# Performance work log

Measured on AMD Instinct MI355X. Metric: run time of the kernel, lower is better.

## Reference

```python
import jax, jax.numpy as jnp
import numpy as np

N = 50000      # nodes
E = 800000     # edges (before self loops)
F_IN = 50      # PPI num_features
H = 4          # heads
C = 64         # hidden per head
NC = 121       # PPI num_classes
NEG_SLOPE = 0.2


def setup_inputs() -> dict:
    key = jax.random.key(0)
    ks = jax.random.split(key, 20)
    p = lambda k, shape: (jax.random.normal(k, shape, jnp.float32) * 0.1)
    x0 = jax.random.normal(ks[0], (N, F_IN), jnp.float32)
    edge_index = jax.random.randint(ks[1], (2, E), 0, N, dtype=jnp.int64)
    return dict(
        x0=x0, edge_index=edge_index,
        W1=p(ks[2], (F_IN, H * C)), as1=p(ks[3], (H, C)), ad1=p(ks[4], (H, C)),
        res1=p(ks[5], (F_IN, H * C)), b1=jnp.zeros((H * C,), jnp.float32),
        W2=p(ks[6], (H * C, H * C)), as2=p(ks[7], (H, C)), ad2=p(ks[8], (H, C)),
        res2=p(ks[9], (H * C, H * C)), b2=jnp.zeros((H * C,), jnp.float32),
        W3=p(ks[10], (H * C, H * NC)), as3=p(ks[11], (H, NC)), ad3=p(ks[12], (H, NC)),
        res3=p(ks[13], (H * C, NC)), b3=jnp.zeros((NC,), jnp.float32),
    )


def _gat(x, src, dst, W, a_src, a_dst, resW, b, concat):
    """PyG-style GATConv with residual, self loops already in (src, dst)."""
    n = x.shape[0]
    heads, outc = a_src.shape
    h = (x @ W).reshape(n, heads, outc)                 # [N,H,C]
    al_s = (h * a_src).sum(-1)                          # [N,H]
    al_d = (h * a_dst).sum(-1)                          # [N,H]
    e = jax.nn.leaky_relu(al_s[src] + al_d[dst], NEG_SLOPE)  # [E,H]
    m = jax.ops.segment_max(e, dst, num_segments=n)     # stable softmax per dst
    ex = jnp.exp(e - m[dst])
    denom = jax.ops.segment_sum(ex, dst, num_segments=n)
    alpha = ex / denom[dst]                             # [E,H]
    out = jax.ops.segment_sum(h[src] * alpha[:, :, None], dst, num_segments=n)  # [N,H,C]
    out = out.reshape(n, heads * outc) if concat else out.mean(axis=1)
    return out + x @ resW + b


def reference(x0, edge_index,
              W1, as1, ad1, res1, b1,
              W2, as2, ad2, res2, b2,
              W3, as3, ad3, res3, b3):
    n = x0.shape[0]
    loop = jnp.arange(n, dtype=edge_index.dtype)        # add self loops (PyG default)
    src = jnp.concatenate([edge_index[0], loop])
    dst = jnp.concatenate([edge_index[1], loop])
    x1 = jax.nn.relu(_gat(x0, src, dst, W1, as1, ad1, res1, b1, True))
    x2 = jax.nn.relu(_gat(x1, src, dst, W2, as2, ad2, res2, b2, True))
    x3 = _gat(x2, src, dst, W3, as3, ad3, res3, b3, False)
    return x3
```

## Files before the change

kernel.cpp:

```cpp
#include <hip/hip_runtime.h>

#define NNODES 50000
#define NEDGES 800000
#define NTOT   (NEDGES + NNODES)
#define F_IN   50
#define KPAD1  64
#define HEADS  4
#define C1     64
#define HC1    256
#define NC     121
#define K1S    320
#define K3S    1280
#define N2S    512
#define SLOTS  128

typedef unsigned short ushort_t;
typedef __attribute__((ext_vector_type(4))) unsigned short ushort4_t;
typedef __attribute__((ext_vector_type(8))) unsigned short ushort8;
typedef __attribute__((ext_vector_type(8))) __bf16 bf16x8;
typedef __attribute__((ext_vector_type(4))) float f32x4;
typedef __attribute__((ext_vector_type(4))) int int4_t;

__device__ __forceinline__ ushort_t f2bf(float f) {
    union { float f; unsigned int u; } v; v.f = f;
    unsigned int u = v.u;
    return (ushort_t)((u + 0x7fffu + ((u >> 16) & 1u)) >> 16);
}
__device__ __forceinline__ float bf2f(ushort_t s) {
    union { unsigned int u; float f; } v; v.u = ((unsigned int)s) << 16;
    return v.f;
}
__device__ __forceinline__ float lrelu(float x) { return x > 0.f ? x : 0.2f * x; }
__device__ __forceinline__ f32x4 cvt4lo(ushort8 v) {
    f32x4 r; r[0] = bf2f(v[0]); r[1] = bf2f(v[1]); r[2] = bf2f(v[2]); r[3] = bf2f(v[3]);
    return r;
}
__device__ __forceinline__ f32x4 cvt4hi(ushort8 v) {
    f32x4 r; r[0] = bf2f(v[4]); r[1] = bf2f(v[5]); r[2] = bf2f(v[6]); r[3] = bf2f(v[7]);
    return r;
}
__device__ __forceinline__ void wave_lds_sync() {
    asm volatile("s_waitcnt lgkmcnt(0)" ::: "memory");
}

__device__ __forceinline__ void scatter_body(int i, const int* __restrict__ ei,
                                             int* __restrict__ cnt,
                                             int* __restrict__ csr_src) {
    if (i >= NTOT) return;
    int s, d;
    if (i < NEDGES) { s = ei[i]; d = ei[NEDGES + i]; }
    else            { s = d = i - NEDGES; }
    if ((unsigned)d >= NNODES) d = 0;
    if ((unsigned)s >= NNODES) s = 0;
    int k = atomicAdd(&cnt[d], 1);
    if (k < SLOTS) csr_src[d * SLOTS + k] = s;
}

#define SZ_A (NNODES * KPAD1)
#define SZ_B (HC1 * K1S)
#define SZ_C (N2S * HC1)
#define SZ_D (N2S)
#define SZ_E (NC * K3S)
#define SZ_F (KPAD1 * 4)
#define SZ_G (HC1 * 4)
#define PREP_TOTAL (SZ_A + SZ_B + SZ_C + SZ_D + SZ_E + 2 * SZ_F + 4 * SZ_G)
#define PREP_BLK ((PREP_TOTAL + 255) / 256)
#define CNT_BLK  ((NTOT + 255) / 256)

__device__ void prep_body(int i,
                 const float* __restrict__ x0,
                 const float* __restrict__ W1, const float* __restrict__ res1,
                 const float* __restrict__ W2, const float* __restrict__ res2,
                 const float* __restrict__ W3, const float* __restrict__ res3,
                 const float* __restrict__ as1, const float* __restrict__ ad1,
                 const float* __restrict__ as2, const float* __restrict__ ad2,
                 const float* __restrict__ as3, const float* __restrict__ ad3,
                 const float* __restrict__ b2,
                 ushort_t* __restrict__ x0b, ushort_t* __restrict__ Bt1,
                 ushort_t* __restrict__ Bt2, ushort_t* __restrict__ Bt3,
                 float* __restrict__ bias512,
                 float* __restrict__ w_as1, float* __restrict__ w_ad1,
                 float* __restrict__ w_as2, float* __restrict__ w_ad2,
                 float* __restrict__ w_as3, float* __restrict__ w_ad3) {
    if (i < SZ_A) {
        int m = i >> 6, k = i & 63;
        x0b[i] = (k < F_IN) ? f2bf(x0[(size_t)m * F_IN + k]) : (ushort_t)0;
        return;
    }
    i -= SZ_A;
    if (i < SZ_B) {
        int c = i / K1S, kk = i - c * K1S;
        float v = 0.f;
        if (kk < 256) {
            int h = kk >> 6, k = kk & 63;
            if (k < F_IN && (c >> 6) == h) v = W1[(size_t)k * HC1 + c];
        } else {
            int k = kk - 256;
            if (k < F_IN) v = res1[(size_t)k * HC1 + c];
        }
        Bt1[i] = f2bf(v);
        return;
    }
    i -= SZ_B;
    if (i < SZ_C) {
        int c = i / HC1, k = i - c * HC1;
        float v = (c < HC1) ? W2[(size_t)k * HC1 + c] : res2[(size_t)k * HC1 + (c - HC1)];
        Bt2[i] = f2bf(v);
        return;
    }
    i -= SZ_C;
    if (i < SZ_D) {
        bias512[i] = (i < HC1) ? 0.f : b2[i - HC1];
        return;
    }
    i -= SZ_D;
    if (i < SZ_E) {
        int c = i / K3S, kk = i - c * K3S;
        float v;
        if (kk < 1024) {
            int h = kk >> 8, k = kk & 255;
            v = 0.25f * W3[(size_t)k * (HEADS * NC) + h * NC + c];
        } else {
            int k = kk - 1024;
            v = res3[(size_t)k * NC + c];
        }
        Bt3[i] = f2bf(v);
        return;
    }
    i -= SZ_E;
    if (i < 2 * SZ_F) {
        const float* a = (i < SZ_F) ? as1 : ad1;
        float* w = (i < SZ_F) ? w_as1 : w_ad1;
        int ii = (i < SZ_F) ? i : i - SZ_F;
        int k = ii >> 2, h = ii & 3;
        float s = 0.f;
        if (k < F_IN)
            for (int c = 0; c < C1; ++c) s += W1[(size_t)k * HC1 + h * C1 + c] * a[h * C1 + c];
        w[ii] = s;
        return;
    }
    i -= 2 * SZ_F;
    {
        int grp = i / SZ_G, ii = i - grp * SZ_G;
        int k = ii >> 2, h = ii & 3;
        float s = 0.f;
        if (grp < 2) {
            const float* a = grp ? ad2 : as2;
            for (int c = 0; c < C1; ++c) s += W2[(size_t)k * HC1 + h * C1 + c] * a[h * C1 + c];
            (grp ? w_ad2 : w_as2)[ii] = s;
        } else {
            const float* a = (grp == 3) ? ad3 : as3;
            for (int c = 0; c < NC; ++c) s += W3[(size_t)k * (HEADS * NC) + h * NC + c] * a[h * NC + c];
            ((grp == 3) ? w_ad3 : w_as3)[ii] = s;
        }
    }
}

__global__ __launch_bounds__(256)
void prep_scatter_kernel(const float* __restrict__ x0,
                 const float* __restrict__ W1, const float* __restrict__ res1,
                 const float* __restrict__ W2, const float* __restrict__ res2,
                 const float* __restrict__ W3, const float* __restrict__ res3,
                 const float* __restrict__ as1, const float* __restrict__ ad1,
                 const float* __restrict__ as2, const float* __restrict__ ad2,
                 const float* __restrict__ as3, const float* __restrict__ ad3,
                 const float* __restrict__ b2,
                 ushort_t* __restrict__ x0b, ushort_t* __restrict__ Bt1,
                 ushort_t* __restrict__ Bt2, ushort_t* __restrict__ Bt3,
                 float* __restrict__ bias512,
                 float* __restrict__ w_as1, float* __restrict__ w_ad1,
                 float* __restrict__ w_as2, float* __restrict__ w_ad2,
                 float* __restrict__ w_as3, float* __restrict__ w_ad3,
                 const int* __restrict__ ei, int* __restrict__ cnt,
                 int* __restrict__ csr_src) {
    int b = blockIdx.x;
    if (b < PREP_BLK) {
        prep_body(b * 256 + threadIdx.x, x0, W1, res1, W2, res2, W3, res3,
                  as1, ad1, as2, ad2, as3, ad3, b2, x0b, Bt1, Bt2, Bt3,
                  bias512, w_as1, w_ad1, w_as2, w_ad2, w_as3, w_ad3);
    } else {
        scatter_body((b - PREP_BLK) * 256 + threadIdx.x, ei, cnt, csr_src);
    }
}

#define BM 128
#define BN 128
#define BK 64
#define LDP (BK + 8)

__global__ __launch_bounds__(256)
void gemm_mfma_kernel(const ushort_t* __restrict__ A1, int lda1,
                      const ushort_t* __restrict__ A2, int lda2, int Ksplit,
                      const ushort_t* __restrict__ Bt, const float* __restrict__ bias,
                      float* __restrict__ Cf, ushort_t* __restrict__ Cb,
                      int M, int N, int K, int relu) {
    __shared__ ushort_t As[BM * LDP];
    __shared__ ushort_t Bs[BN * LDP];
    int tid = threadIdx.x;
    int lane = tid & 63;
    int wid = tid >> 6;
    int wm = (wid & 1) * 64, wn = (wid >> 1) * 64;
    int l15 = lane & 15;
    int q8 = (lane >> 4) * 8;
    int m0 = blockIdx.y * BM, n0 = blockIdx.x * BN;

    f32x4 acc[4][4] = {};

    for (int k0 = 0; k0 < K; k0 += BK) {
        #pragma unroll
        for (int it = 0; it < 4; ++it) {
            int c = tid + it * 256;
            int row = c >> 3, c8 = c & 7;
            int k = k0 + c8 * 8;
            ushort8 va = (ushort8)0;
            int gm = m0 + row;
            if (gm < M) {
                if (k < Ksplit) va = *(const ushort8*)&A1[(size_t)gm * lda1 + k];
                else            va = *(const ushort8*)&A2[(size_t)gm * lda2 + (k - Ksplit)];
            }
            *(ushort8*)&As[row * LDP + c8 * 8] = va;
            ushort8 vb = (ushort8)0;
            int gn = n0 + row;
            if (gn < N) vb = *(const ushort8*)&Bt[(size_t)gn * K + k];
            *(ushort8*)&Bs[row * LDP + c8 * 8] = vb;
        }
        __syncthreads();
        #pragma unroll
        for (int kk = 0; kk < BK; kk += 32) {
            bf16x8 af[4], bfr[4];
            #pragma unroll
            for (int mi = 0; mi < 4; ++mi)
                af[mi] = *(const bf16x8*)&As[(wm + mi * 16 + l15) * LDP + kk + q8];
            #pragma unroll
            for (int ni = 0; ni < 4; ++ni)
                bfr[ni] = *(const bf16x8*)&Bs[(wn + ni * 16 + l15) * LDP + kk + q8];
            #pragma unroll
            for (int mi = 0; mi < 4; ++mi)
                #pragma unroll
                for (int ni = 0; ni < 4; ++ni)
                    acc[mi][ni] = __builtin_amdgcn_mfma_f32_16x16x32_bf16(
                        af[mi], bfr[ni], acc[mi][ni], 0, 0, 0);
        }
        __syncthreads();
    }

    #pragma unroll
    for (int mi = 0; mi < 4; ++mi) {
        int mbase = m0 + wm + mi * 16 + (lane >> 4) * 4;
        #pragma unroll
        for (int ni = 0; ni < 4; ++ni) {
            int ncol = n0 + wn + ni * 16 + l15;
            if (ncol >= N) continue;
            float bv = bias ? bias[ncol] : 0.f;
            #pragma unroll
            for (int r = 0; r < 4; ++r) {
                int m = mbase + r;
                if (m >= M) continue;
                float v = acc[mi][ni][r] + bv;
                if (relu) v = fmaxf(v, 0.f);
                if (Cf) Cf[(size_t)m * N + ncol] = v;
                else    Cb[(size_t)m * N + ncol] = f2bf(v);
            }
        }
    }
}

__global__ __launch_bounds__(256)
void gemm3s_kernel(const ushort_t* __restrict__ A1, int lda1,
                   const ushort_t* __restrict__ A2, int lda2, int Ksplit,
                   const ushort_t* __restrict__ Bt, const float* __restrict__ bias,
                   float* __restrict__ out, int M, int N, int K) {
    __shared__ ushort_t As[64 * LDP];
    __shared__ ushort_t Bs[128 * LDP];
    int tid = threadIdx.x, lane = tid & 63, wid = tid >> 6;
    int l15 = lane & 15, q8 = (lane >> 4) * 8;
    int m0 = blockIdx.x * 64;
    f32x4 c4[8] = {};
    for (int k0 = 0; k0 < K; k0 += BK) {
        #pragma unroll
        for (int it = 0; it < 2; ++it) {
            int c = tid + it * 256;
            int row = c >> 3, c8 = c & 7;
            int k = k0 + c8 * 8;
            ushort8 va = (ushort8)0;
            int gm = m0 + row;
            if (gm < M) {
                if (k < Ksplit) va = *(const ushort8*)&A1[(size_t)gm * lda1 + k];
                else            va = *(const ushort8*)&A2[(size_t)gm * lda2 + (k - Ksplit)];
            }
            *(ushort8*)&As[row * LDP + c8 * 8] = va;
        }
        #pragma unroll
        for (int it = 0; it < 4; ++it) {
            int c = tid + it * 256;
            int row = c >> 3, c8 = c & 7;
            int k = k0 + c8 * 8;
            ushort8 vb = (ushort8)0;
            if (row < N) vb = *(const ushort8*)&Bt[(size_t)row * K + k];
            *(ushort8*)&Bs[row * LDP + c8 * 8] = vb;
        }
        __syncthreads();
        #pragma unroll
        for (int kk = 0; kk < BK; kk += 32) {
            bf16x8 af = *(const bf16x8*)&As[(wid * 16 + l15) * LDP + kk + q8];
            #pragma unroll
            for (int ni = 0; ni < 8; ++ni) {
                bf16x8 bf = *(const bf16x8*)&Bs[(ni * 16 + l15) * LDP + kk + q8];
                c4[ni] = __builtin_amdgcn_mfma_f32_16x16x32_bf16(af, bf, c4[ni], 0, 0, 0);
            }
        }
        __syncthreads();
    }
    int rbase = m0 + wid * 16 + (lane >> 4) * 4;
    #pragma unroll
    for (int ni = 0; ni < 8; ++ni) {
        int col = ni * 16 + l15;
        if (col >= NC) continue;
        float bv = bias[col];
        #pragma unroll
        for (int r = 0; r < 4; ++r) {
            int m = rbase + r;
            if (m < M) out[(size_t)m * NC + col] = c4[ni][r] + bv;
        }
    }
}

__global__ __launch_bounds__(256)
void logits_gemv_kernel(const ushort_t* __restrict__ X, int K,
                        const float* __restrict__ w_as, const float* __restrict__ w_ad,
                        float* __restrict__ als, float* __restrict__ ald) {
    int wid = threadIdx.x >> 6, lane = threadIdx.x & 63;
    int n = blockIdx.x * 4 + wid;
    float ps[HEADS] = {}, pd[HEADS] = {};
    for (int k0 = lane * 4; k0 < K; k0 += 256) {
        ushort4_t xv = *(const ushort4_t*)&X[(size_t)n * K + k0];
        float x[4] = {bf2f(xv.x), bf2f(xv.y), bf2f(xv.z), bf2f(xv.w)};
        #pragma unroll
        for (int j = 0; j < 4; ++j) {
            #pragma unroll
            for (int h = 0; h < HEADS; ++h) {
                ps[h] += x[j] * w_as[(k0 + j) * 4 + h];
                pd[h] += x[j] * w_ad[(k0 + j) * 4 + h];
            }
        }
    }
    #pragma unroll
    for (int off = 32; off; off >>= 1)
        #pragma unroll
        for (int h = 0; h < HEADS; ++h) {
            ps[h] += __shfl_xor(ps[h], off);
            pd[h] += __shfl_xor(pd[h], off);
        }
    if (lane == 0)
        #pragma unroll
        for (int h = 0; h < HEADS; ++h) {
            als[n * HEADS + h] = ps[h];
            ald[n * HEADS + h] = pd[h];
        }
}

#define E_CHUNK32(ROWBYTES)                                                   \
    int i = base + l;                                                         \
    int nv = end - base; if (nv > 32) nv = 32;                                \
    if (i < end) {                                                            \
        int s = csr_src[i];                                                   \
        soffw[l] = s * (ROWBYTES);                                            \
        f32x4 av = *(const f32x4*)&als[s * 4];                                \
        f32x4 e;                                                              \
        _Pragma("unroll")                                                     \
        for (int h = 0; h < HEADS; ++h) {                                     \
            e[h] = __expf(lrelu(av[h] + aldd[h]));                            \
            den4[h] += e[h];                                                  \
        }                                                                     \
        *(f32x4*)&sew[l * 4] = e;                                             \
    }                                                                         \
    wave_lds_sync();

#define DEN_REDUCE16                                                          \
    _Pragma("unroll")                                                         \
    for (int off = 16; off; off >>= 1)                                        \
        _Pragma("unroll")                                                     \
        for (int h = 0; h < HEADS; ++h)                                       \
            den4[h] += __shfl_xor(den4[h], off);

__global__ __launch_bounds__(256)
void agg1_kernel(const ushort_t* __restrict__ x0b,
                 const float* __restrict__ als, const float* __restrict__ ald,
                 const int* __restrict__ cnt, const int* __restrict__ csr_src,
                 ushort_t* __restrict__ aggx) {
    __shared__ int   soff[8][32];
    __shared__ float se[8][32 * 4];
    int tid = threadIdx.x;
    int hw = tid >> 5, l = tid & 31;
    int d = blockIdx.x * 8 + hw;
    int* soffw = soff[hw];
    float* sew = se[hw];
    int beg = d * SLOTS;
    int deg = cnt[d]; if (deg > SLOTS) deg = SLOTS;
    int end = beg + deg;
    f32x4 aldd = *(const f32x4*)&ald[d * 4];
    f32x4 den4 = (f32x4)0.f;
    f32x4 acc0 = (f32x4)0.f, acc1 = (f32x4)0.f;
    int lb = l * 4;
    for (int base = beg; base < end; base += 32) {
        E_CHUNK32(KPAD1 * 2)
        int j = 0;
        for (; j + 4 <= nv; j += 4) {
            int4_t o = *(const int4_t*)&soffw[j];
            f32x4 e0 = *(const f32x4*)&sew[j * 4];
            f32x4 e1 = *(const f32x4*)&sew[(j + 1) * 4];
            f32x4 e2 = *(const f32x4*)&sew[(j + 2) * 4];
            f32x4 e3 = *(const f32x4*)&sew[(j + 3) * 4];
            unsigned int v0 = *(const unsigned int*)((const char*)x0b + o.x + lb);
            unsigned int v1 = *(const unsigned int*)((const char*)x0b + o.y + lb);
            unsigned int v2 = *(const unsigned int*)((const char*)x0b + o.z + lb);
            unsigned int v3 = *(const unsigned int*)((const char*)x0b + o.w + lb);
            acc0 += e0 * bf2f((ushort_t)(v0 & 0xffffu)) + e1 * bf2f((ushort_t)(v1 & 0xffffu))
                  + e2 * bf2f((ushort_t)(v2 & 0xffffu)) + e3 * bf2f((ushort_t)(v3 & 0xffffu));
            acc1 += e0 * bf2f((ushort_t)(v0 >> 16)) + e1 * bf2f((ushort_t)(v1 >> 16))
                  + e2 * bf2f((ushort_t)(v2 >> 16)) + e3 * bf2f((ushort_t)(v3 >> 16));
        }
        for (; j < nv; ++j) {
            int o = soffw[j];
            f32x4 e = *(const f32x4*)&sew[j * 4];
            unsigned int v = *(const unsigned int*)((const char*)x0b + o + lb);
            acc0 += e * bf2f((ushort_t)(v & 0xffffu));
            acc1 += e * bf2f((ushort_t)(v >> 16));
        }
        wave_lds_sync();
    }
    DEN_REDUCE16
    #pragma unroll
    for (int h = 0; h < HEADS; ++h) {
        float r = 1.f / den4[h];
        unsigned int pk = (unsigned int)f2bf(acc0[h] * r)
                        | ((unsigned int)f2bf(acc1[h] * r) << 16);
        *(unsigned int*)&aggx[(size_t)d * HC1 + h * 64 + l * 2] = pk;
    }
}

__global__ __launch_bounds__(256)
void agg2_kernel(const ushort_t* __restrict__ comb,
                 const float* __restrict__ als, const float* __restrict__ ald,
                 const int* __restrict__ cnt, const int* __restrict__ csr_src,
                 const float* __restrict__ w_as3, const float* __restrict__ w_ad3,
                 ushort_t* __restrict__ xnext,
                 float* __restrict__ als3, float* __restrict__ ald3) {
    __shared__ int   soff[8][32];
    __shared__ float se[8][32 * 4];
    int tid = threadIdx.x;
    int hw = tid >> 5, l = tid & 31;
    int d = blockIdx.x * 8 + hw;
    int* soffw = soff[hw];
    float* sew = se[hw];
    int hh = l >> 3;
    int beg = d * SLOTS;
    int deg = cnt[d]; if (deg > SLOTS) deg = SLOTS;
    int end = beg + deg;
    f32x4 aldd = *(const f32x4*)&ald[d * 4];
    f32x4 den4 = (f32x4)0.f;
    f32x4 acc[2] = {};
    int lb = l * 16;
    for (int base = beg; base < end; base += 32) {
        E_CHUNK32(N2S * 2)
        int j = 0;
        for (; j + 4 <= nv; j += 4) {
            int4_t o = *(const int4_t*)&soffw[j];
            ushort8 v0 = *(const ushort8*)((const char*)comb + o.x + lb);
            ushort8 v1 = *(const ushort8*)((const char*)comb + o.y + lb);
            ushort8 v2 = *(const ushort8*)((const char*)comb + o.z + lb);
            ushort8 v3 = *(const ushort8*)((const char*)comb + o.w + lb);
            float e0 = sew[j * 4 + hh], e1 = sew[(j + 1) * 4 + hh];
            float e2 = sew[(j + 2) * 4 + hh], e3 = sew[(j + 3) * 4 + hh];
            acc[0] += e0 * cvt4lo(v0) + e1 * cvt4lo(v1) + e2 * cvt4lo(v2) + e3 * cvt4lo(v3);
            acc[1] += e0 * cvt4hi(v0) + e1 * cvt4hi(v1) + e2 * cvt4hi(v2) + e3 * cvt4hi(v3);
        }
        for (; j < nv; ++j) {
            int o = soffw[j];
            float e = sew[j * 4 + hh];
            ushort8 v = *(const ushort8*)((const char*)comb + o + lb);
            acc[0] += e * cvt4lo(v);
            acc[1] += e * cvt4hi(v);
        }
        wave_lds_sync();
    }
    DEN_REDUCE16
    float r = 1.f / den4[hh];
    ushort8 rv = *(const ushort8*)&comb[(size_t)d * N2S + 256 + l * 8];
    float vout[8];
    ushort8 o8;
    #pragma unroll
    for (int q = 0; q < 2; ++q)
        #pragma unroll
        for (int c = 0; c < 4; ++c) {
            float vv = fmaxf(acc[q][c] * r + bf2f(rv[q * 4 + c]), 0.f);
            vout[q * 4 + c] = vv;
            o8[q * 4 + c] = f2bf(vv);
        }
    *(ushort8*)&xnext[(size_t)d * HC1 + l * 8] = o8;
    f32x4 ps = (f32x4)0.f, pd = (f32x4)0.f;
    #pragma unroll
    for (int cc = 0; cc < 8; ++cc) {
        int col = l * 8 + cc;
        f32x4 wsj = *(const f32x4*)&w_as3[col * 4];
        f32x4 wdj = *(const f32x4*)&w_ad3[col * 4];
        ps += vout[cc] * wsj;
        pd += vout[cc] * wdj;
    }
    #pragma unroll
    for (int off = 16; off; off >>= 1) {
        #pragma unroll
        for (int h = 0; h < HEADS; ++h) {
            ps[h] += __shfl_xor(ps[h], off);
            pd[h] += __shfl_xor(pd[h], off);
        }
    }
    if (l == 0) {
        *(f32x4*)&als3[d * 4] = ps;
        *(f32x4*)&ald3[d * 4] = pd;
    }
}

__global__ __launch_bounds__(256)
void agg3_kernel(const ushort_t* __restrict__ x2b,
                 const float* __restrict__ als, const float* __restrict__ ald,
                 const int* __restrict__ cnt, const int* __restrict__ csr_src,
                 ushort_t* __restrict__ aggx) {
    __shared__ int   soff[8][32];
    __shared__ float se[8][32 * 4];
    int tid = threadIdx.x;
    int hw = tid >> 5, l = tid & 31;
    int d = blockIdx.x * 8 + hw;
    int* soffw = soff[hw];
    float* sew = se[hw];
    int beg = d * SLOTS;
    int deg = cnt[d]; if (deg > SLOTS) deg = SLOTS;
    int end = beg + deg;
    f32x4 aldd = *(const f32x4*)&ald[d * 4];
    f32x4 den4 = (f32x4)0.f;
    f32x4 acc[HEADS][2] = {};
    int lb = l * 16;
    for (int base = beg; base < end; base += 32) {
        E_CHUNK32(HC1 * 2)
        int j = 0;
        for (; j + 4 <= nv; j += 4) {
            int4_t o = *(const int4_t*)&soffw[j];
            ushort8 v0 = *(const ushort8*)((const char*)x2b + o.x + lb);
            ushort8 v1 = *(const ushort8*)((const char*)x2b + o.y + lb);
            ushort8 v2 = *(const ushort8*)((const char*)x2b + o.z + lb);
            ushort8 v3 = *(const ushort8*)((const char*)x2b + o.w + lb);
            f32x4 e0 = *(const f32x4*)&sew[j * 4];
            f32x4 e1 = *(const f32x4*)&sew[(j + 1) * 4];
            f32x4 e2 = *(const f32x4*)&sew[(j + 2) * 4];
            f32x4 e3 = *(const f32x4*)&sew[(j + 3) * 4];
            f32x4 xl, xh;
            xl = cvt4lo(v0); xh = cvt4hi(v0);
            #pragma unroll
            for (int h = 0; h < HEADS; ++h) { acc[h][0] += e0[h] * xl; acc[h][1] += e0[h] * xh; }
            xl = cvt4lo(v1); xh = cvt4hi(v1);
            #pragma unroll
            for (int h = 0; h < HEADS; ++h) { acc[h][0] += e1[h] * xl; acc[h][1] += e1[h] * xh; }
            xl = cvt4lo(v2); xh = cvt4hi(v2);
            #pragma unroll
            for (int h = 0; h < HEADS; ++h) { acc[h][0] += e2[h] * xl; acc[h][1] += e2[h] * xh; }
            xl = cvt4lo(v3); xh = cvt4hi(v3);
            #pragma unroll
            for (int h = 0; h < HEADS; ++h) { acc[h][0] += e3[h] * xl; acc[h][1] += e3[h] * xh; }
        }
        for (; j < nv; ++j) {
            int o = soffw[j];
            f32x4 e = *(const f32x4*)&sew[j * 4];
            ushort8 v = *(const ushort8*)((const char*)x2b + o + lb);
            f32x4 xl = cvt4lo(v), xh = cvt4hi(v);
            #pragma unroll
            for (int h = 0; h < HEADS; ++h) { acc[h][0] += e[h] * xl; acc[h][1] += e[h] * xh; }
        }
        wave_lds_sync();
    }
    DEN_REDUCE16
    #pragma unroll
    for (int h = 0; h < HEADS; ++h) {
        float rdv = 1.f / den4[h];
        ushort8 ow;
        #pragma unroll
        for (int q = 0; q < 2; ++q)
            #pragma unroll
            for (int c = 0; c < 4; ++c)
                ow[q * 4 + c] = f2bf(acc[h][q][c] * rdv);
        *(ushort8*)&aggx[(size_t)d * 1024 + h * HC1 + l * 8] = ow;
    }
}

extern "C" void kernel_launch(void* const* d_in, const int* in_sizes, int n_in,
                              void* d_out, int out_size, void* d_ws, size_t ws_size,
                              hipStream_t stream) {
    const float* x0   = (const float*)d_in[0];
    const int*   ei   = (const int*)d_in[1];
    const float* W1   = (const float*)d_in[2];
    const float* as1  = (const float*)d_in[3];
    const float* ad1  = (const float*)d_in[4];
    const float* res1 = (const float*)d_in[5];
    const float* b1   = (const float*)d_in[6];
    const float* W2   = (const float*)d_in[7];
    const float* as2  = (const float*)d_in[8];
    const float* ad2  = (const float*)d_in[9];
    const float* res2 = (const float*)d_in[10];
    const float* b2   = (const float*)d_in[11];
    const float* W3   = (const float*)d_in[12];
    const float* as3  = (const float*)d_in[13];
    const float* ad3  = (const float*)d_in[14];
    const float* res3 = (const float*)d_in[15];
    const float* b3   = (const float*)d_in[16];

    char* p = (char*)d_ws;
    auto alloc = [&](size_t bytes) -> void* {
        void* r = (void*)p;
        p += (bytes + 255) & ~(size_t)255;
        return r;
    };
    int*      cnt     = (int*)alloc((size_t)NNODES * 4);
    int*      csr_src = (int*)alloc((size_t)NNODES * SLOTS * 4);
    float*    als     = (float*)alloc((size_t)NNODES * HEADS * 4);
    float*    ald     = (float*)alloc((size_t)NNODES * HEADS * 4);
    float*    als3    = (float*)alloc((size_t)NNODES * HEADS * 4);
    float*    ald3    = (float*)alloc((size_t)NNODES * HEADS * 4);
    ushort_t* x0b     = (ushort_t*)alloc((size_t)NNODES * KPAD1 * 2);
    ushort_t* x2      = (ushort_t*)alloc((size_t)NNODES * HC1 * 2);
    ushort_t* Bt1     = (ushort_t*)alloc((size_t)HC1 * K1S * 2);
    ushort_t* Bt2     = (ushort_t*)alloc((size_t)N2S * HC1 * 2);
    float*    bias512 = (float*)alloc((size_t)N2S * 4);
    ushort_t* Bt3     = (ushort_t*)alloc((size_t)NC * K3S * 2);
    float*    w_as1   = (float*)alloc((size_t)KPAD1 * 4 * 4);
    float*    w_ad1   = (float*)alloc((size_t)KPAD1 * 4 * 4);
    float*    w_as2   = (float*)alloc((size_t)HC1 * 4 * 4);
    float*    w_ad2   = (float*)alloc((size_t)HC1 * 4 * 4);
    float*    w_as3   = (float*)alloc((size_t)HC1 * 4 * 4);
    float*    w_ad3   = (float*)alloc((size_t)HC1 * 4 * 4);
    char*     big     = (char*)alloc((size_t)NNODES * 1024 * 2);
    ushort_t* aggx1   = (ushort_t*)big;
    ushort_t* x1      = (ushort_t*)(big + (size_t)NNODES * HC1 * 2);
    ushort_t* comb    = (ushort_t*)(big + (size_t)NNODES * HC1 * 4);
    ushort_t* aggx3   = (ushort_t*)big;

    hipMemsetAsync(cnt, 0, (size_t)NNODES * 4, stream);

    prep_scatter_kernel<<<PREP_BLK + CNT_BLK, 256, 0, stream>>>(
        x0, W1, res1, W2, res2, W3, res3, as1, ad1, as2, ad2, as3, ad3, b2,
        x0b, Bt1, Bt2, Bt3, bias512, w_as1, w_ad1, w_as2, w_ad2, w_as3, w_ad3,
        ei, cnt, csr_src);

    auto gemm = [&](const ushort_t* A1, int lda1, const ushort_t* A2, int lda2, int Ksplit,
                    const ushort_t* Bt, const float* bias,
                    float* Cf, ushort_t* Cb, int M, int Nn, int K, int relu) {
        dim3 g((Nn + BN - 1) / BN, (M + BM - 1) / BM);
        gemm_mfma_kernel<<<g, 256, 0, stream>>>(A1, lda1, A2, lda2, Ksplit, Bt, bias,
                                                Cf, Cb, M, Nn, K, relu);
    };

    int nagg4 = NNODES / 4;
    int nagg8 = NNODES / 8;

    logits_gemv_kernel<<<nagg4, 256, 0, stream>>>(x0b, KPAD1, w_as1, w_ad1, als, ald);
    agg1_kernel<<<nagg8, 256, 0, stream>>>(x0b, als, ald, cnt, csr_src, aggx1);
    gemm(aggx1, HC1, x0b, KPAD1, HC1, Bt1, b1, nullptr, x1, NNODES, HC1, K1S, 1);

    gemm(x1, HC1, x1, HC1, HC1, Bt2, bias512, nullptr, comb, NNODES, N2S, HC1, 0);
    logits_gemv_kernel<<<nagg4, 256, 0, stream>>>(x1, HC1, w_as2, w_ad2, als, ald);
    agg2_kernel<<<nagg8, 256, 0, stream>>>(comb, als, ald, cnt, csr_src,
                                           w_as3, w_ad3, x2, als3, ald3);

    agg3_kernel<<<nagg8, 256, 0, stream>>>(x2, als3, ald3, cnt, csr_src, aggx3);
    gemm3s_kernel<<<(NNODES + 63) / 64, 256, 0, stream>>>(
        aggx3, 1024, x2, HC1, 1024, Bt3, b3, (float*)d_out, NNODES, 128, K3S);
}
```

Measured before the change: 591.5 us.

## Split layer-2/3 aggregation into column stripes with edges spread across lanes

The layer-2 and layer-3 aggregation kernels now launch eight blocks per group of nodes. Each block handles a 32-column stripe, and the lanes of a half-wave split into 8 edge groups of 4 column lanes, with a shuffle reduction at the end. This is meant to raise parallelism and memory-level concurrency for gathered rows. The price is recomputing the per-edge softmax weights eight times, extra shuffles, and a new partial-logit buffer plus a small reduce kernel to build the layer-3 attention logits.

```diff
diff --git a/kernel.cpp b/kernel.cpp
--- a/kernel.cpp
+++ b/kernel.cpp
@@ -440,97 +440,117 @@
 }
 
 __global__ __launch_bounds__(256)
-void agg2_kernel(const ushort_t* __restrict__ comb,
-                 const float* __restrict__ als, const float* __restrict__ ald,
-                 const int* __restrict__ cnt, const int* __restrict__ csr_src,
-                 const float* __restrict__ w_as3, const float* __restrict__ w_ad3,
-                 ushort_t* __restrict__ xnext,
-                 float* __restrict__ als3, float* __restrict__ ald3) {
+void agg2s_kernel(const ushort_t* __restrict__ comb,
+                  const float* __restrict__ als, const float* __restrict__ ald,
+                  const int* __restrict__ cnt, const int* __restrict__ csr_src,
+                  const float* __restrict__ w_as3, const float* __restrict__ w_ad3,
+                  ushort_t* __restrict__ xnext, float* __restrict__ pbuf) {
     __shared__ int   soff[8][32];
     __shared__ float se[8][32 * 4];
     int tid = threadIdx.x;
     int hw = tid >> 5, l = tid & 31;
-    int d = blockIdx.x * 8 + hw;
+    int gb = blockIdx.x;
+    int stripe = gb & 7;
+    int d = (gb >> 3) * 8 + hw;
     int* soffw = soff[hw];
     float* sew = se[hw];
-    int hh = l >> 3;
+    int hh = stripe >> 1;
     int beg = d * SLOTS;
     int deg = cnt[d]; if (deg > SLOTS) deg = SLOTS;
     int end = beg + deg;
     f32x4 aldd = *(const f32x4*)&ald[d * 4];
     f32x4 den4 = (f32x4)0.f;
     f32x4 acc[2] = {};
-    int lb = l * 16;
+    int cg = l & 3;
+    int eg = l >> 2;
+    int lb = stripe * 64 + cg * 16;
     for (int base = beg; base < end; base += 32) {
         E_CHUNK32(N2S * 2)
-        int j = 0;
-        for (; j + 4 <= nv; j += 4) {
-            int4_t o = *(const int4_t*)&soffw[j];
-            ushort8 v0 = *(const ushort8*)((const char*)comb + o.x + lb);
-            ushort8 v1 = *(const ushort8*)((const char*)comb + o.y + lb);
-            ushort8 v2 = *(const ushort8*)((const char*)comb + o.z + lb);
-            ushort8 v3 = *(const ushort8*)((const char*)comb + o.w + lb);
-            float e0 = sew[j * 4 + hh], e1 = sew[(j + 1) * 4 + hh];
-            float e2 = sew[(j + 2) * 4 + hh], e3 = sew[(j + 3) * 4 + hh];
-            acc[0] += e0 * cvt4lo(v0) + e1 * cvt4lo(v1) + e2 * cvt4lo(v2) + e3 * cvt4lo(v3);
-            acc[1] += e0 * cvt4hi(v0) + e1 * cvt4hi(v1) + e2 * cvt4hi(v2) + e3 * cvt4hi(v3);
-        }
-        for (; j < nv; ++j) {
-            int o = soffw[j];
-            float e = sew[j * 4 + hh];
-            ushort8 v = *(const ushort8*)((const char*)comb + o + lb);
-            acc[0] += e * cvt4lo(v);
-            acc[1] += e * cvt4hi(v);
+        for (int j = 0; j < nv; j += 8) {
+            int le = j + eg;
+            if (le < nv) {
+                int o = soffw[le];
+                float e = sew[le * 4 + hh];
+                ushort8 v = *(const ushort8*)((const char*)comb + o + lb);
+                acc[0] += e * cvt4lo(v);
+                acc[1] += e * cvt4hi(v);
+            }
         }
         wave_lds_sync();
     }
     DEN_REDUCE16
-    float r = 1.f / den4[hh];
-    ushort8 rv = *(const ushort8*)&comb[(size_t)d * N2S + 256 + l * 8];
-    float vout[8];
-    ushort8 o8;
     #pragma unroll
-    for (int q = 0; q < 2; ++q)
-        #pragma unroll
-        for (int c = 0; c < 4; ++c) {
-            float vv = fmaxf(acc[q][c] * r + bf2f(rv[q * 4 + c]), 0.f);
-            vout[q * 4 + c] = vv;
-            o8[q * 4 + c] = f2bf(vv);
-        }
-    *(ushort8*)&xnext[(size_t)d * HC1 + l * 8] = o8;
+    for (int off = 4; off <= 16; off <<= 1)
+        #pragma unroll
+        for (int q = 0; q < 2; ++q)
+            #pragma unroll
+            for (int c = 0; c < 4; ++c)
+                acc[q][c] += __shfl_xor(acc[q][c], off);
+    if (eg == 0) {
+        float r = 1.f / den4[hh];
+        ushort8 rv = *(const ushort8*)&comb[(size_t)d * N2S + 256 + stripe * 32 + cg * 8];
+        float vout[8];
+        ushort8 o8;
+        #pragma unroll
+        for (int q = 0; q < 2; ++q)
+            #pragma unroll
+            for (int c = 0; c < 4; ++c) {
+                float vv = fmaxf(acc[q][c] * r + bf2f(rv[q * 4 + c]), 0.f);
+                vout[q * 4 + c] = vv;
+                o8[q * 4 + c] = f2bf(vv);
+            }
+        *(ushort8*)&xnext[(size_t)d * HC1 + stripe * 32 + cg * 8] = o8;
+        f32x4 ps = (f32x4)0.f, pd = (f32x4)0.f;
+        #pragma unroll
+        for (int cc = 0; cc < 8; ++cc) {
+            int col = stripe * 32 + cg * 8 + cc;
+            ps += vout[cc] * (*(const f32x4*)&w_as3[col * 4]);
+            pd += vout[cc] * (*(const f32x4*)&w_ad3[col * 4]);
+        }
+        #pragma unroll
+        for (int off = 1; off <= 2; off <<= 1) {
+            #pragma unroll
+            for (int h = 0; h < HEADS; ++h) {
+                ps[h] += __shfl_xor(ps[h], off);
+                pd[h] += __shfl_xor(pd[h], off);
+            }
+        }
+        if (cg == 0) {
+            float* pb = &pbuf[((size_t)stripe * NNODES + d) * 8];
+            *(f32x4*)pb = ps;
+            *(f32x4*)(pb + 4) = pd;
+        }
+    }
+}
+
+__global__ __launch_bounds__(256)
+void logits3_reduce_kernel(const float* __restrict__ pbuf,
+                           float* __restrict__ als3, float* __restrict__ ald3) {
+    int d = blockIdx.x * 256 + threadIdx.x;
+    if (d >= NNODES) return;
     f32x4 ps = (f32x4)0.f, pd = (f32x4)0.f;
     #pragma unroll
-    for (int cc = 0; cc < 8; ++cc) {
-        int col = l * 8 + cc;
-        f32x4 wsj = *(const f32x4*)&w_as3[col * 4];
-        f32x4 wdj = *(const f32x4*)&w_ad3[col * 4];
-        ps += vout[cc] * wsj;
-        pd += vout[cc] * wdj;
-    }
-    #pragma unroll
-    for (int off = 16; off; off >>= 1) {
-        #pragma unroll
-        for (int h = 0; h < HEADS; ++h) {
-            ps[h] += __shfl_xor(ps[h], off);
-            pd[h] += __shfl_xor(pd[h], off);
-        }
-    }
-    if (l == 0) {
-        *(f32x4*)&als3[d * 4] = ps;
-        *(f32x4*)&ald3[d * 4] = pd;
-    }
-}
-
-__global__ __launch_bounds__(256)
-void agg3_kernel(const ushort_t* __restrict__ x2b,
-                 const float* __restrict__ als, const float* __restrict__ ald,
-                 const int* __restrict__ cnt, const int* __restrict__ csr_src,
-                 ushort_t* __restrict__ aggx) {
+    for (int s = 0; s < 8; ++s) {
+        const float* pb = &pbuf[((size_t)s * NNODES + d) * 8];
+        ps += *(const f32x4*)pb;
+        pd += *(const f32x4*)(pb + 4);
+    }
+    *(f32x4*)&als3[d * 4] = ps;
+    *(f32x4*)&ald3[d * 4] = pd;
+}
+
+__global__ __launch_bounds__(256)
+void agg3s_kernel(const ushort_t* __restrict__ x2b,
+                  const float* __restrict__ als, const float* __restrict__ ald,
+                  const int* __restrict__ cnt, const int* __restrict__ csr_src,
+                  ushort_t* __restrict__ aggx) {
     __shared__ int   soff[8][32];
     __shared__ float se[8][32 * 4];
     int tid = threadIdx.x;
     int hw = tid >> 5, l = tid & 31;
-    int d = blockIdx.x * 8 + hw;
+    int gb = blockIdx.x;
+    int stripe = gb & 7;
+    int d = (gb >> 3) * 8 + hw;
     int* soffw = soff[hw];
     float* sew = se[hw];
     int beg = d * SLOTS;
@@ -539,55 +559,49 @@
     f32x4 aldd = *(const f32x4*)&ald[d * 4];
     f32x4 den4 = (f32x4)0.f;
     f32x4 acc[HEADS][2] = {};
-    int lb = l * 16;
+    int cg = l & 3;
+    int eg = l >> 2;
+    int lb = stripe * 64 + cg * 16;
     for (int base = beg; base < end; base += 32) {
         E_CHUNK32(HC1 * 2)
-        int j = 0;
-        for (; j + 4 <= nv; j += 4) {
-            int4_t o = *(const int4_t*)&soffw[j];
-            ushort8 v0 = *(const ushort8*)((const char*)x2b + o.x + lb);
-            ushort8 v1 = *(const ushort8*)((const char*)x2b + o.y + lb);
-            ushort8 v2 = *(const ushort8*)((const char*)x2b + o.z + lb);
-            ushort8 v3 = *(const ushort8*)((const char*)x2b + o.w + lb);
-            f32x4 e0 = *(const f32x4*)&sew[j * 4];
-            f32x4 e1 = *(const f32x4*)&sew[(j + 1) * 4];
-            f32x4 e2 = *(const f32x4*)&sew[(j + 2) * 4];
-            f32x4 e3 = *(const f32x4*)&sew[(j + 3) * 4];
-            f32x4 xl, xh;
-            xl = cvt4lo(v0); xh = cvt4hi(v0);
-            #pragma unroll
-            for (int h = 0; h < HEADS; ++h) { acc[h][0] += e0[h] * xl; acc[h][1] += e0[h] * xh; }
-            xl = cvt4lo(v1); xh = cvt4hi(v1);
-            #pragma unroll
-            for (int h = 0; h < HEADS; ++h) { acc[h][0] += e1[h] * xl; acc[h][1] += e1[h] * xh; }
-            xl = cvt4lo(v2); xh = cvt4hi(v2);
-            #pragma unroll
-            for (int h = 0; h < HEADS; ++h) { acc[h][0] += e2[h] * xl; acc[h][1] += e2[h] * xh; }
-            xl = cvt4lo(v3); xh = cvt4hi(v3);
-            #pragma unroll
-            for (int h = 0; h < HEADS; ++h) { acc[h][0] += e3[h] * xl; acc[h][1] += e3[h] * xh; }
-        }
-        for (; j < nv; ++j) {
-            int o = soffw[j];
-            f32x4 e = *(const f32x4*)&sew[j * 4];
-            ushort8 v = *(const ushort8*)((const char*)x2b + o + lb);
-            f32x4 xl = cvt4lo(v), xh = cvt4hi(v);
-            #pragma unroll
-            for (int h = 0; h < HEADS; ++h) { acc[h][0] += e[h] * xl; acc[h][1] += e[h] * xh; }
+        for (int j = 0; j < nv; j += 8) {
+            int le = j + eg;
+            if (le < nv) {
+                int o = soffw[le];
+                f32x4 e = *(const f32x4*)&sew[le * 4];
+                ushort8 v = *(const ushort8*)((const char*)x2b + o + lb);
+                f32x4 xl = cvt4lo(v), xh = cvt4hi(v);
+                #pragma unroll
+                for (int h = 0; h < HEADS; ++h) {
+                    acc[h][0] += e[h] * xl;
+                    acc[h][1] += e[h] * xh;
+                }
+            }
         }
         wave_lds_sync();
     }
     DEN_REDUCE16
     #pragma unroll
-    for (int h = 0; h < HEADS; ++h) {
-        float rdv = 1.f / den4[h];
-        ushort8 ow;
-        #pragma unroll
-        for (int q = 0; q < 2; ++q)
-            #pragma unroll
-            for (int c = 0; c < 4; ++c)
-                ow[q * 4 + c] = f2bf(acc[h][q][c] * rdv);
-        *(ushort8*)&aggx[(size_t)d * 1024 + h * HC1 + l * 8] = ow;
+    for (int off = 4; off <= 16; off <<= 1)
+        #pragma unroll
+        for (int h = 0; h < HEADS; ++h)
+            #pragma unroll
+            for (int q = 0; q < 2; ++q)
+                #pragma unroll
+                for (int c = 0; c < 4; ++c)
+                    acc[h][q][c] += __shfl_xor(acc[h][q][c], off);
+    if (eg == 0) {
+        #pragma unroll
+        for (int h = 0; h < HEADS; ++h) {
+            float rdv = 1.f / den4[h];
+            ushort8 ow;
+            #pragma unroll
+            for (int q = 0; q < 2; ++q)
+                #pragma unroll
+                for (int c = 0; c < 4; ++c)
+                    ow[q * 4 + c] = f2bf(acc[h][q][c] * rdv);
+            *(ushort8*)&aggx[(size_t)d * 1024 + h * HC1 + stripe * 32 + cg * 8] = ow;
+        }
     }
 }
 
@@ -624,6 +638,7 @@
     float*    ald     = (float*)alloc((size_t)NNODES * HEADS * 4);
     float*    als3    = (float*)alloc((size_t)NNODES * HEADS * 4);
     float*    ald3    = (float*)alloc((size_t)NNODES * HEADS * 4);
+    float*    pbuf    = (float*)alloc((size_t)8 * NNODES * 8 * 4);
     ushort_t* x0b     = (ushort_t*)alloc((size_t)NNODES * KPAD1 * 2);
     ushort_t* x2      = (ushort_t*)alloc((size_t)NNODES * HC1 * 2);
     ushort_t* Bt1     = (ushort_t*)alloc((size_t)HC1 * K1S * 2);
@@ -659,6 +674,7 @@
 
     int nagg4 = NNODES / 4;
     int nagg8 = NNODES / 8;
+    int nstrp = (NNODES / 8) * 8;
 
     logits_gemv_kernel<<<nagg4, 256, 0, stream>>>(x0b, KPAD1, w_as1, w_ad1, als, ald);
     agg1_kernel<<<nagg8, 256, 0, stream>>>(x0b, als, ald, cnt, csr_src, aggx1);
@@ -666,10 +682,11 @@
 
     gemm(x1, HC1, x1, HC1, HC1, Bt2, bias512, nullptr, comb, NNODES, N2S, HC1, 0);
     logits_gemv_kernel<<<nagg4, 256, 0, stream>>>(x1, HC1, w_as2, w_ad2, als, ald);
-    agg2_kernel<<<nagg8, 256, 0, stream>>>(comb, als, ald, cnt, csr_src,
-                                           w_as3, w_ad3, x2, als3, ald3);
-
-    agg3_kernel<<<nagg8, 256, 0, stream>>>(x2, als3, ald3, cnt, csr_src, aggx3);
+    agg2s_kernel<<<nstrp, 256, 0, stream>>>(comb, als, ald, cnt, csr_src,
+                                            w_as3, w_ad3, x2, pbuf);
+    logits3_reduce_kernel<<<(NNODES + 255) / 256, 256, 0, stream>>>(pbuf, als3, ald3);
+
+    agg3s_kernel<<<nstrp, 256, 0, stream>>>(x2, als3, ald3, cnt, csr_src, aggx3);
     gemm3s_kernel<<<(NNODES + 63) / 64, 256, 0, stream>>>(
         aggx3, 1024, x2, HC1, 1024, Bt3, b3, (float*)d_out, NNODES, 128, K3S);
 }
```

After: 864.4 us. +46.1%, slower.

## Fold attention logit GEMVs into prep kernel and extended layer-2 GEMM

Applied to the files above, without the earlier changes.

Removes the two standalone logits_gemv launches. The layer-1 logits are now computed inside the prep/scatter kernel from fp32 x0, with weights precomputed into LDS. The layer-2 logits become 8 extra output columns of the layer-2 GEMM (N padded from 512 to 520), so they come straight from the MFMA accumulators. The edge scatter also processes 4 edges per thread. The extra columns add a fifth, mostly empty N-tile to the layer-2 GEMM, and each prep-side GEMV block recomputes the W1·a weight products.

```diff
diff --git a/kernel.cpp b/kernel.cpp
--- a/kernel.cpp
+++ b/kernel.cpp
@@ -12,6 +12,7 @@
 #define K1S    320
 #define K3S    1280
 #define N2S    512
+#define N2X    520
 #define SLOTS  128
 
 typedef unsigned short ushort_t;
@@ -43,44 +44,45 @@
     asm volatile("s_waitcnt lgkmcnt(0)" ::: "memory");
 }
 
-__device__ __forceinline__ void scatter_body(int i, const int* __restrict__ ei,
-                                             int* __restrict__ cnt,
-                                             int* __restrict__ csr_src) {
-    if (i >= NTOT) return;
-    int s, d;
-    if (i < NEDGES) { s = ei[i]; d = ei[NEDGES + i]; }
-    else            { s = d = i - NEDGES; }
-    if ((unsigned)d >= NNODES) d = 0;
-    if ((unsigned)s >= NNODES) s = 0;
-    int k = atomicAdd(&cnt[d], 1);
-    if (k < SLOTS) csr_src[d * SLOTS + k] = s;
+__device__ __forceinline__ void scatter_body4(int i0, const int* __restrict__ ei,
+                                              int* __restrict__ cnt,
+                                              int* __restrict__ csr_src) {
+    #pragma unroll
+    for (int u = 0; u < 4; ++u) {
+        int i = i0 + u * 256;
+        if (i >= NTOT) continue;
+        int s, d;
+        if (i < NEDGES) { s = ei[i]; d = ei[NEDGES + i]; }
+        else            { s = d = i - NEDGES; }
+        if ((unsigned)d >= NNODES) d = 0;
+        if ((unsigned)s >= NNODES) s = 0;
+        int k = atomicAdd(&cnt[d], 1);
+        if (k < SLOTS) csr_src[d * SLOTS + k] = s;
+    }
 }
 
 #define SZ_A (NNODES * KPAD1)
 #define SZ_B (HC1 * K1S)
-#define SZ_C (N2S * HC1)
-#define SZ_D (N2S)
+#define SZ_C (N2X * HC1)
+#define SZ_D (N2X)
 #define SZ_E (NC * K3S)
-#define SZ_F (KPAD1 * 4)
 #define SZ_G (HC1 * 4)
-#define PREP_TOTAL (SZ_A + SZ_B + SZ_C + SZ_D + SZ_E + 2 * SZ_F + 4 * SZ_G)
+#define PREP_TOTAL (SZ_A + SZ_B + SZ_C + SZ_D + SZ_E + 2 * SZ_G)
 #define PREP_BLK ((PREP_TOTAL + 255) / 256)
-#define CNT_BLK  ((NTOT + 255) / 256)
+#define SCAT_BLK ((NTOT + 1023) / 1024)
+#define GEMV1_BLK (NNODES / 8)
 
 __device__ void prep_body(int i,
                  const float* __restrict__ x0,
                  const float* __restrict__ W1, const float* __restrict__ res1,
                  const float* __restrict__ W2, const float* __restrict__ res2,
                  const float* __restrict__ W3, const float* __restrict__ res3,
-                 const float* __restrict__ as1, const float* __restrict__ ad1,
                  const float* __restrict__ as2, const float* __restrict__ ad2,
                  const float* __restrict__ as3, const float* __restrict__ ad3,
                  const float* __restrict__ b2,
                  ushort_t* __restrict__ x0b, ushort_t* __restrict__ Bt1,
                  ushort_t* __restrict__ Bt2, ushort_t* __restrict__ Bt3,
-                 float* __restrict__ bias512,
-                 float* __restrict__ w_as1, float* __restrict__ w_ad1,
-                 float* __restrict__ w_as2, float* __restrict__ w_ad2,
+                 float* __restrict__ bias520,
                  float* __restrict__ w_as3, float* __restrict__ w_ad3) {
     if (i < SZ_A) {
         int m = i >> 6, k = i & 63;
@@ -104,13 +106,26 @@
     i -= SZ_B;
     if (i < SZ_C) {
         int c = i / HC1, k = i - c * HC1;
-        float v = (c < HC1) ? W2[(size_t)k * HC1 + c] : res2[(size_t)k * HC1 + (c - HC1)];
+        float v;
+        if (c < HC1) {
+            v = W2[(size_t)k * HC1 + c];
+        } else if (c < 512) {
+            v = res2[(size_t)k * HC1 + (c - HC1)];
+        } else {
+            int j = c - 512;
+            int h = j & 3;
+            const float* a = (j < 4) ? as2 : ad2;
+            float s = 0.f;
+            for (int cc = 0; cc < C1; ++cc)
+                s += W2[(size_t)k * HC1 + h * C1 + cc] * a[h * C1 + cc];
+            v = s;
+        }
         Bt2[i] = f2bf(v);
         return;
     }
     i -= SZ_C;
     if (i < SZ_D) {
-        bias512[i] = (i < HC1) ? 0.f : b2[i - HC1];
+        bias520[i] = (i >= HC1 && i < 512) ? b2[i - HC1] : 0.f;
         return;
     }
     i -= SZ_D;
@@ -128,36 +143,59 @@
         return;
     }
     i -= SZ_E;
-    if (i < 2 * SZ_F) {
-        const float* a = (i < SZ_F) ? as1 : ad1;
-        float* w = (i < SZ_F) ? w_as1 : w_ad1;
-        int ii = (i < SZ_F) ? i : i - SZ_F;
-        int k = ii >> 2, h = ii & 3;
-        float s = 0.f;
-        if (k < F_IN)
-            for (int c = 0; c < C1; ++c) s += W1[(size_t)k * HC1 + h * C1 + c] * a[h * C1 + c];
-        w[ii] = s;
-        return;
-    }
-    i -= 2 * SZ_F;
     {
         int grp = i / SZ_G, ii = i - grp * SZ_G;
         int k = ii >> 2, h = ii & 3;
+        const float* a = grp ? ad3 : as3;
         float s = 0.f;
-        if (grp < 2) {
-            const float* a = grp ? ad2 : as2;
-            for (int c = 0; c < C1; ++c) s += W2[(size_t)k * HC1 + h * C1 + c] * a[h * C1 + c];
-            (grp ? w_ad2 : w_as2)[ii] = s;
-        } else {
-            const float* a = (grp == 3) ? ad3 : as3;
-            for (int c = 0; c < NC; ++c) s += W3[(size_t)k * (HEADS * NC) + h * NC + c] * a[h * NC + c];
-            ((grp == 3) ? w_ad3 : w_as3)[ii] = s;
+        for (int c = 0; c < NC; ++c)
+            s += W3[(size_t)k * (HEADS * NC) + h * NC + c] * a[h * NC + c];
+        (grp ? w_ad3 : w_as3)[ii] = s;
+    }
+}
+
+__device__ void gemv1_body(int b, int tid,
+                           const float* __restrict__ x0,
+                           const float* __restrict__ W1,
+                           const float* __restrict__ as1, const float* __restrict__ ad1,
+                           float* __restrict__ als, float* __restrict__ ald,
+                           float* lds_w ) {
+    int k = tid >> 2, h = tid & 3;
+    float s = 0.f, sd = 0.f;
+    if (k < F_IN) {
+        for (int c = 0; c < C1; ++c) {
+            float wv = W1[(size_t)k * HC1 + h * C1 + c];
+            s  += wv * as1[h * C1 + c];
+            sd += wv * ad1[h * C1 + c];
+        }
+    }
+    lds_w[k * 8 + h] = s;
+    lds_w[k * 8 + 4 + h] = sd;
+    __syncthreads();
+    int wid = tid >> 6, lane = tid & 63;
+    #pragma unroll
+    for (int t = 0; t < 2; ++t) {
+        int n = b * 8 + wid * 2 + t;
+        float xv = (lane < F_IN) ? x0[(size_t)n * F_IN + lane] : 0.f;
+        f32x4 was = *(const f32x4*)&lds_w[lane * 8];
+        f32x4 wad = *(const f32x4*)&lds_w[lane * 8 + 4];
+        f32x4 ps = xv * was, pd = xv * wad;
+        #pragma unroll
+        for (int off = 32; off; off >>= 1)
+            #pragma unroll
+            for (int hh = 0; hh < HEADS; ++hh) {
+                ps[hh] += __shfl_xor(ps[hh], off);
+                pd[hh] += __shfl_xor(pd[hh], off);
+            }
+        if (lane == 0) {
+            *(f32x4*)&als[n * 4] = ps;
+            *(f32x4*)&ald[n * 4] = pd;
         }
     }
 }
 
 __global__ __launch_bounds__(256)
-void prep_scatter_kernel(const float* __restrict__ x0,
+void prep_scatter_gemv_kernel(const float* __restrict__ x0,
                  const float* __restrict__ W1, const float* __restrict__ res1,
                  const float* __restrict__ W2, const float* __restrict__ res2,
                  const float* __restrict__ W3, const float* __restrict__ res3,
@@ -167,19 +205,22 @@
                  const float* __restrict__ b2,
                  ushort_t* __restrict__ x0b, ushort_t* __restrict__ Bt1,
                  ushort_t* __restrict__ Bt2, ushort_t* __restrict__ Bt3,
-                 float* __restrict__ bias512,
-                 float* __restrict__ w_as1, float* __restrict__ w_ad1,
-                 float* __restrict__ w_as2, float* __restrict__ w_ad2,
+                 float* __restrict__ bias520,
                  float* __restrict__ w_as3, float* __restrict__ w_ad3,
                  const int* __restrict__ ei, int* __restrict__ cnt,
-                 int* __restrict__ csr_src) {
+                 int* __restrict__ csr_src,
+                 float* __restrict__ als, float* __restrict__ ald) {
+    __shared__ float lds_w[64 * 8];
     int b = blockIdx.x;
     if (b < PREP_BLK) {
         prep_body(b * 256 + threadIdx.x, x0, W1, res1, W2, res2, W3, res3,
-                  as1, ad1, as2, ad2, as3, ad3, b2, x0b, Bt1, Bt2, Bt3,
-                  bias512, w_as1, w_ad1, w_as2, w_ad2, w_as3, w_ad3);
+                  as2, ad2, as3, ad3, b2, x0b, Bt1, Bt2, Bt3,
+                  bias520, w_as3, w_ad3);
+    } else if (b < PREP_BLK + SCAT_BLK) {
+        scatter_body4((b - PREP_BLK) * 1024 + threadIdx.x, ei, cnt, csr_src);
     } else {
-        scatter_body((b - PREP_BLK) * 256 + threadIdx.x, ei, cnt, csr_src);
+        gemv1_body(b - PREP_BLK - SCAT_BLK, threadIdx.x, x0, W1, as1, ad1,
+                   als, ald, lds_w);
     }
 }
 
@@ -192,7 +233,7 @@
 void gemm_mfma_kernel(const ushort_t* __restrict__ A1, int lda1,
                       const ushort_t* __restrict__ A2, int lda2, int Ksplit,
                       const ushort_t* __restrict__ Bt, const float* __restrict__ bias,
-                      float* __restrict__ Cf, ushort_t* __restrict__ Cb,
+                      ushort_t* __restrict__ Cb,
                       int M, int N, int K, int relu) {
     __shared__ ushort_t As[BM * LDP];
     __shared__ ushort_t Bs[BN * LDP];
@@ -258,8 +299,86 @@
                 if (m >= M) continue;
                 float v = acc[mi][ni][r] + bv;
                 if (relu) v = fmaxf(v, 0.f);
-                if (Cf) Cf[(size_t)m * N + ncol] = v;
-                else    Cb[(size_t)m * N + ncol] = f2bf(v);
+                Cb[(size_t)m * N + ncol] = f2bf(v);
+            }
+        }
+    }
+}
+
+__global__ __launch_bounds__(256)
+void gemm2x_kernel(const ushort_t* __restrict__ A,
+                   const ushort_t* __restrict__ Bt,
+                   const float* __restrict__ bias,
+                   ushort_t* __restrict__ comb,
+                   float* __restrict__ als, float* __restrict__ ald,
+                   int M) {
+    __shared__ ushort_t As[BM * LDP];
+    __shared__ ushort_t Bs[BN * LDP];
+    int tid = threadIdx.x;
+    int lane = tid & 63;
+    int wid = tid >> 6;
+    int wm = (wid & 1) * 64, wn = (wid >> 1) * 64;
+    int l15 = lane & 15;
+    int q8 = (lane >> 4) * 8;
+    int m0 = blockIdx.y * BM, n0 = blockIdx.x * BN;
+
+    f32x4 acc[4][4] = {};
+
+    for (int k0 = 0; k0 < HC1; k0 += BK) {
+        #pragma unroll
+        for (int it = 0; it < 4; ++it) {
+            int c = tid + it * 256;
+            int row = c >> 3, c8 = c & 7;
+            int k = k0 + c8 * 8;
+            ushort8 va = (ushort8)0;
+            int gm = m0 + row;
+            if (gm < M) va = *(const ushort8*)&A[(size_t)gm * HC1 + k];
+            *(ushort8*)&As[row * LDP + c8 * 8] = va;
+            ushort8 vb = (ushort8)0;
+            int gn = n0 + row;
+            if (gn < N2X) vb = *(const ushort8*)&Bt[(size_t)gn * HC1 + k];
+            *(ushort8*)&Bs[row * LDP + c8 * 8] = vb;
+        }
+        __syncthreads();
+        #pragma unroll
+        for (int kk = 0; kk < BK; kk += 32) {
+            bf16x8 af[4], bfr[4];
+            #pragma unroll
+            for (int mi = 0; mi < 4; ++mi)
+                af[mi] = *(const bf16x8*)&As[(wm + mi * 16 + l15) * LDP + kk + q8];
+            #pragma unroll
+            for (int ni = 0; ni < 4; ++ni)
+                bfr[ni] = *(const bf16x8*)&Bs[(wn + ni * 16 + l15) * LDP + kk + q8];
+            #pragma unroll
+            for (int mi = 0; mi < 4; ++mi)
+                #pragma unroll
+                for (int ni = 0; ni < 4; ++ni)
+                    acc[mi][ni] = __builtin_amdgcn_mfma_f32_16x16x32_bf16(
+                        af[mi], bfr[ni], acc[mi][ni], 0, 0, 0);
+        }
+        __syncthreads();
+    }
+
+    #pragma unroll
+    for (int mi = 0; mi < 4; ++mi) {
+        int mbase = m0 + wm + mi * 16 + (lane >> 4) * 4;
+        #pragma unroll
+        for (int ni = 0; ni < 4; ++ni) {
+            int ncol = n0 + wn + ni * 16 + l15;
+            if (ncol >= N2X) continue;
+            float bv = bias[ncol];
+            #pragma unroll
+            for (int r = 0; r < 4; ++r) {
+                int m = mbase + r;
+                if (m >= M) continue;
+                float v = acc[mi][ni][r] + bv;
+                if (ncol < 512) {
+                    comb[(size_t)m * N2S + ncol] = f2bf(v);
+                } else {
+                    int j = ncol - 512;
+                    if (j < 4) als[m * 4 + j] = v;
+                    else       ald[m * 4 + (j - 4)] = v;
+                }
             }
         }
     }
@@ -323,40 +442,6 @@
             if (m < M) out[(size_t)m * NC + col] = c4[ni][r] + bv;
         }
     }
-}
-
-__global__ __launch_bounds__(256)
-void logits_gemv_kernel(const ushort_t* __restrict__ X, int K,
-                        const float* __restrict__ w_as, const float* __restrict__ w_ad,
-                        float* __restrict__ als, float* __restrict__ ald) {
-    int wid = threadIdx.x >> 6, lane = threadIdx.x & 63;
-    int n = blockIdx.x * 4 + wid;
-    float ps[HEADS] = {}, pd[HEADS] = {};
-    for (int k0 = lane * 4; k0 < K; k0 += 256) {
-        ushort4_t xv = *(const ushort4_t*)&X[(size_t)n * K + k0];
-        float x[4] = {bf2f(xv.x), bf2f(xv.y), bf2f(xv.z), bf2f(xv.w)};
-        #pragma unroll
-        for (int j = 0; j < 4; ++j) {
-            #pragma unroll
-            for (int h = 0; h < HEADS; ++h) {
-                ps[h] += x[j] * w_as[(k0 + j) * 4 + h];
-                pd[h] += x[j] * w_ad[(k0 + j) * 4 + h];
-            }
-        }
-    }
-    #pragma unroll
-    for (int off = 32; off; off >>= 1)
-        #pragma unroll
-        for (int h = 0; h < HEADS; ++h) {
-            ps[h] += __shfl_xor(ps[h], off);
-            pd[h] += __shfl_xor(pd[h], off);
-        }
-    if (lane == 0)
-        #pragma unroll
-        for (int h = 0; h < HEADS; ++h) {
-            als[n * HEADS + h] = ps[h];
-            ald[n * HEADS + h] = pd[h];
-        }
 }
 
 #define E_CHUNK32(ROWBYTES)                                                   \
@@ -627,13 +712,9 @@
     ushort_t* x0b     = (ushort_t*)alloc((size_t)NNODES * KPAD1 * 2);
     ushort_t* x2      = (ushort_t*)alloc((size_t)NNODES * HC1 * 2);
     ushort_t* Bt1     = (ushort_t*)alloc((size_t)HC1 * K1S * 2);
-    ushort_t* Bt2     = (ushort_t*)alloc((size_t)N2S * HC1 * 2);
-    float*    bias512 = (float*)alloc((size_t)N2S * 4);
+    ushort_t* Bt2     = (ushort_t*)alloc((size_t)N2X * HC1 * 2);
+    float*    bias520 = (float*)alloc((size_t)N2X * 4);
     ushort_t* Bt3     = (ushort_t*)alloc((size_t)NC * K3S * 2);
-    float*    w_as1   = (float*)alloc((size_t)KPAD1 * 4 * 4);
-    float*    w_ad1   = (float*)alloc((size_t)KPAD1 * 4 * 4);
-    float*    w_as2   = (float*)alloc((size_t)HC1 * 4 * 4);
-    float*    w_ad2   = (float*)alloc((size_t)HC1 * 4 * 4);
     float*    w_as3   = (float*)alloc((size_t)HC1 * 4 * 4);
     float*    w_ad3   = (float*)alloc((size_t)HC1 * 4 * 4);
     char*     big     = (char*)alloc((size_t)NNODES * 1024 * 2);
@@ -644,28 +725,24 @@
 
     hipMemsetAsync(cnt, 0, (size_t)NNODES * 4, stream);
 
-    prep_scatter_kernel<<<PREP_BLK + CNT_BLK, 256, 0, stream>>>(
+    prep_scatter_gemv_kernel<<<PREP_BLK + SCAT_BLK + GEMV1_BLK, 256, 0, stream>>>(
         x0, W1, res1, W2, res2, W3, res3, as1, ad1, as2, ad2, as3, ad3, b2,
-        x0b, Bt1, Bt2, Bt3, bias512, w_as1, w_ad1, w_as2, w_ad2, w_as3, w_ad3,
-        ei, cnt, csr_src);
-
-    auto gemm = [&](const ushort_t* A1, int lda1, const ushort_t* A2, int lda2, int Ksplit,
-                    const ushort_t* Bt, const float* bias,
-                    float* Cf, ushort_t* Cb, int M, int Nn, int K, int relu) {
-        dim3 g((Nn + BN - 1) / BN, (M + BM - 1) / BM);
-        gemm_mfma_kernel<<<g, 256, 0, stream>>>(A1, lda1, A2, lda2, Ksplit, Bt, bias,
-                                                Cf, Cb, M, Nn, K, relu);
-    };
-
-    int nagg4 = NNODES / 4;
+        x0b, Bt1, Bt2, Bt3, bias520, w_as3, w_ad3,
+        ei, cnt, csr_src, als, ald);
+
     int nagg8 = NNODES / 8;
 
-    logits_gemv_kernel<<<nagg4, 256, 0, stream>>>(x0b, KPAD1, w_as1, w_ad1, als, ald);
     agg1_kernel<<<nagg8, 256, 0, stream>>>(x0b, als, ald, cnt, csr_src, aggx1);
-    gemm(aggx1, HC1, x0b, KPAD1, HC1, Bt1, b1, nullptr, x1, NNODES, HC1, K1S, 1);
-
-    gemm(x1, HC1, x1, HC1, HC1, Bt2, bias512, nullptr, comb, NNODES, N2S, HC1, 0);
-    logits_gemv_kernel<<<nagg4, 256, 0, stream>>>(x1, HC1, w_as2, w_ad2, als, ald);
+    {
+        dim3 g((HC1 + BN - 1) / BN, (NNODES + BM - 1) / BM);
+        gemm_mfma_kernel<<<g, 256, 0, stream>>>(aggx1, HC1, x0b, KPAD1, HC1,
+                                                Bt1, b1, x1, NNODES, HC1, K1S, 1);
+    }
+
+    {
+        dim3 g((N2X + BN - 1) / BN, (NNODES + BM - 1) / BM);
+        gemm2x_kernel<<<g, 256, 0, stream>>>(x1, Bt2, bias520, comb, als, ald, NNODES);
+    }
     agg2_kernel<<<nagg8, 256, 0, stream>>>(comb, als, ald, cnt, csr_src,
                                            w_as3, w_ad3, x2, als3, ald3);
 
```

New measurement: 623.2 us. 5.4% more time.
